# Kernel optimization log

Measured on AMD Instinct MI355X. Metric: run time of the kernel, lower is better.

The kernel has to match this reference:

```python
import jax, jax.numpy as jnp
import numpy as np

N = 100000
E = 1600000
IN, H, OUT = 128, 128, 64


def setup_inputs() -> dict:
    key = jax.random.key(0)
    k1, k2, k3, k4, k5, k6 = jax.random.split(key, 6)
    x = jax.random.normal(k1, (N, IN), dtype=jnp.float32)
    edge_index = jax.random.randint(k2, (2, E), 0, N, dtype=jnp.int64)
    W1 = jax.random.normal(k3, (IN, H), dtype=jnp.float32) / np.sqrt(IN)
    b1 = jnp.zeros((H,), dtype=jnp.float32)
    W2 = jax.random.normal(k4, (H, OUT), dtype=jnp.float32) / np.sqrt(H)
    b2 = jnp.zeros((OUT,), dtype=jnp.float32)
    return {"x": x, "edge_index": edge_index, "W1": W1, "b1": b1, "W2": W2, "b2": b2}


def gcn_conv(x, src, dst, W, b, num_nodes):
    # PyG GCNConv: linear transform, then symmetric-normalized aggregation
    h = x @ W                                         # (N, d_out)
    ones = jnp.ones(src.shape[0], dtype=h.dtype)
    deg = jax.ops.segment_sum(ones, dst, num_segments=num_nodes)  # in-degree incl. self-loops
    dis = jax.lax.rsqrt(jnp.maximum(deg, 1.0))        # deg >= 1 due to self-loops
    norm = dis[src] * dis[dst]                        # (E+N,)
    msg = h[src] * norm[:, None]                      # gather + scale (memory-bound)
    out = jax.ops.segment_sum(msg, dst, num_segments=num_nodes)
    return out + b


def reference(x, edge_index, W1, b1, W2, b2):
    loop = jnp.arange(N, dtype=edge_index.dtype)
    src = jnp.concatenate([edge_index[0], loop])
    dst = jnp.concatenate([edge_index[1], loop])
    h = gcn_conv(x, src, dst, W1, b1, N)
    h = jax.nn.relu(h)                                # dropout: eval mode (identity)
    out = gcn_conv(h, src, dst, W2, b2, N)
    return jax.nn.sigmoid(out) * 0.8 + 0.1
```

## Files before the change

### kernel.cpp

```cpp
#include <hip/hip_runtime.h>
#include <cstdint>
#include <cstddef>

#define IN_F 128
#define HID  128
#define OUTF 64

typedef unsigned int   uint32;
typedef unsigned short ushort16;

using frag_ab = __attribute__((ext_vector_type(8))) short;
using frag_cd = __attribute__((ext_vector_type(4))) float;

static constexpr int TPB = 256;
static constexpr int PT_TILE = 2048;
static constexpr int PT_EPT  = 8;
static constexpr int MAXBK   = 512;
static constexpr int MEGA_SMEM = 34816;

__device__ __forceinline__ float bflo(uint32 u) { return __uint_as_float(u << 16); }
__device__ __forceinline__ float bfhi(uint32 u) { return __uint_as_float(u & 0xFFFF0000u); }
__device__ __forceinline__ ushort16 f2bf(float f) {
    uint32 x = __float_as_uint(f);
    x = (x + 0x7FFFu + ((x >> 16) & 1u)) >> 16;
    return (ushort16)x;
}
__device__ __forceinline__ uint32 packbf(float a, float b) {
    return (uint32)f2bf(a) | ((uint32)f2bf(b) << 16);
}

__global__ void detect_i64_kernel(const uint32* __restrict__ p, int npairs, int* __restrict__ flag) {
    __shared__ int anynz;
    if (threadIdx.x == 0) anynz = 0;
    __syncthreads();
    int i = threadIdx.x;
    if (i < npairs && p[2 * i + 1] != 0u) atomicOr(&anynz, 1);
    __syncthreads();
    if (threadIdx.x == 0) *flag = (anynz == 0) ? 1 : 0;
}

__device__ __forceinline__ int load_idx(const void* p, int i, bool i64) {
    return i64 ? (int)((const long long*)p)[i] : ((const int*)p)[i];
}

__device__ void partition_body(char* smem, const void* __restrict__ ei, int E, bool i64,
                               int nbuckets, int bcap,
                               int* __restrict__ bcur, uint32* __restrict__ bbuf)
{
    uint32*   stash  = (uint32*)smem;
    ushort16* bidx   = (ushort16*)(smem + 8192);
    int*      hist   = (int*)(smem + 12288);
    int*      scanb  = (int*)(smem + 14336);
    int*      gbase  = (int*)(smem + 16384);
    int*      sum256 = (int*)(smem + 18432);

    int tile0 = blockIdx.x * PT_TILE;
    int tid = threadIdx.x;

    for (int i = tid; i < nbuckets; i += 256) hist[i] = 0;
    __syncthreads();

    uint32 pck[PT_EPT];
    int    lofs[PT_EPT];
    short  bkt[PT_EPT];
#pragma unroll
    for (int j = 0; j < PT_EPT; ++j) {
        int e = tile0 + j * 256 + tid;
        if (e < E) {
            int s = load_idx(ei, e, i64);
            int d = load_idx(ei, E + e, i64);
            int b = d >> 8;
            pck[j]  = (uint32)s | ((uint32)(d & 255) << 24);
            bkt[j]  = (short)b;
            lofs[j] = atomicAdd(&hist[b], 1);
        } else bkt[j] = -1;
    }
    __syncthreads();

    for (int i = tid; i < nbuckets; i += 256)
        gbase[i] = hist[i] ? atomicAdd(&bcur[i], hist[i]) : 0;

    {
        int lt = tid * 2;
        int h0 = 0, h1 = 0;
        if (lt + 0 < nbuckets) h0 = hist[lt + 0];
        if (lt + 1 < nbuckets) h1 = hist[lt + 1];
        int lsum = h0 + h1;
        sum256[tid] = lsum;
        __syncthreads();
        for (int off = 1; off < 256; off <<= 1) {
            int t = (tid >= off) ? sum256[tid - off] : 0;
            __syncthreads();
            sum256[tid] += t;
            __syncthreads();
        }
        int excl = sum256[tid] - lsum;
        if (lt + 0 < nbuckets) scanb[lt + 0] = excl;
        if (lt + 1 < nbuckets) scanb[lt + 1] = excl + h0;
    }
    __syncthreads();

#pragma unroll
    for (int j = 0; j < PT_EPT; ++j) {
        if (bkt[j] >= 0) {
            int p = scanb[bkt[j]] + lofs[j];
            stash[p] = pck[j];
            bidx[p]  = (ushort16)bkt[j];
        }
    }
    __syncthreads();

    int total = min(PT_TILE, E - tile0);
    for (int k = tid; k < total; k += 256) {
        int b = bidx[k];
        int dst = gbase[b] + (k - scanb[b]);
        if (dst < bcap) bbuf[(size_t)b * bcap + dst] = stash[k];
    }
}

__device__ void gemm1_body(char* smem, int gb, const float* __restrict__ X,
                           const float* __restrict__ W, ushort16* __restrict__ out, int M)
{
    typedef ushort16 WtRow[136];
    WtRow* Wt = (WtRow*)smem;

    for (int i = threadIdx.x; i < 128 * 128; i += 256) {
        int k = i >> 7, c = i & 127;
        Wt[c][k] = f2bf(W[i]);
    }
    __syncthreads();

    int wid  = threadIdx.x >> 6;
    int lane = threadIdx.x & 63;
    int g    = lane >> 4;
    int li   = lane & 15;

    int row = gb * 64 + wid * 16 + li;
    int rc  = min(row, M - 1);

    frag_cd acc[8];
#pragma unroll
    for (int i = 0; i < 8; ++i) acc[i] = (frag_cd)0.0f;

#pragma unroll
    for (int t = 0; t < 4; ++t) {
        const float* xp = X + (size_t)rc * 128 + t * 32 + g * 8;
        float4 p = *(const float4*)xp;
        float4 q = *(const float4*)(xp + 4);
        frag_ab a;
        a[0] = (short)f2bf(p.x); a[1] = (short)f2bf(p.y);
        a[2] = (short)f2bf(p.z); a[3] = (short)f2bf(p.w);
        a[4] = (short)f2bf(q.x); a[5] = (short)f2bf(q.y);
        a[6] = (short)f2bf(q.z); a[7] = (short)f2bf(q.w);
#pragma unroll
        for (int cb = 0; cb < 8; ++cb) {
            frag_ab b = *(const frag_ab*)&Wt[cb * 16 + li][t * 32 + g * 8];
            acc[cb] = __builtin_amdgcn_mfma_f32_16x16x32_bf16(a, b, acc[cb], 0, 0, 0);
        }
    }

    int ro = gb * 64 + wid * 16 + g * 4;
#pragma unroll
    for (int r = 0; r < 4; ++r) {
        int rr = ro + r;
        if (rr < M) {
#pragma unroll
            for (int cb = 0; cb < 8; ++cb)
                out[(size_t)rr * 128 + cb * 16 + li] = f2bf(acc[cb][r]);
        }
    }
}

__global__ __launch_bounds__(256) void mega1_kernel(
    const void* __restrict__ ei, int E, const int* __restrict__ flag,
    int nbuckets, int bcap, int* __restrict__ bcur, uint32* __restrict__ bbuf,
    const float* __restrict__ X, const float* __restrict__ W1,
    ushort16* __restrict__ H, int M, int PB)
{
    __shared__ char smem[MEGA_SMEM];
    if ((int)blockIdx.x < PB) {
        partition_body(smem, ei, E, (*flag != 0), nbuckets, bcap, bcur, bbuf);
    } else {
        gemm1_body(smem, blockIdx.x - PB, X, W1, H, M);
    }
}

__global__ void bucket_base_kernel(const int* __restrict__ bcur, int* __restrict__ bbase,
                                   int nbuckets, int bcap) {
    __shared__ int tmp[512];
    int tid = threadIdx.x;
    int v = (tid < nbuckets) ? min(bcur[tid], bcap) : 0;
    tmp[tid] = v;
    __syncthreads();
    for (int off = 1; off < 512; off <<= 1) {
        int t = (tid >= off) ? tmp[tid - off] : 0;
        __syncthreads();
        tmp[tid] += t;
        __syncthreads();
    }
    if (tid < nbuckets) bbase[tid] = tmp[tid] - v;
}

__global__ __launch_bounds__(256) void bucket_count2_kernel(
    const uint32* __restrict__ bbuf, const int* __restrict__ bcur, const int* __restrict__ bbase,
    int* __restrict__ counts, float* __restrict__ dis, int* __restrict__ row_ptr,
    int N, int bcap)
{
    __shared__ int h[256];
    __shared__ int sc[256];
    int tid = threadIdx.x;
    h[tid] = 0;
    __syncthreads();
    int b = blockIdx.x;
    int cnt = min(bcur[b], bcap);
    const uint32* src = bbuf + (size_t)b * bcap;
    for (int k = tid; k < cnt; k += 256) atomicAdd(&h[src[k] >> 24], 1);
    __syncthreads();
    int v = h[tid];
    sc[tid] = v;
    __syncthreads();
    for (int off = 1; off < 256; off <<= 1) {
        int t = (tid >= off) ? sc[tid - off] : 0;
        __syncthreads();
        sc[tid] += t;
        __syncthreads();
    }
    int node = (b << 8) + tid;
    if (node < N) {
        counts[node]  = v;
        dis[node]     = rsqrtf((float)(v + 1));
        row_ptr[node] = bbase[b] + sc[tid] - v;
    }
}

__global__ __launch_bounds__(256) void bucket_fill_kernel(
    const uint32* __restrict__ bbuf, const int* __restrict__ bcur,
    const int* __restrict__ row_ptr, int* __restrict__ csr, int N, int bcap)
{
    __shared__ int cur[256];
    int b = blockIdx.x;
    int node = (b << 8) + threadIdx.x;
    cur[threadIdx.x] = (node < N) ? row_ptr[node] : 0;
    __syncthreads();
    int cnt = min(bcur[b], bcap);
    const uint32* src = bbuf + (size_t)b * bcap;
    for (int k = threadIdx.x; k < cnt; k += 256) {
        uint32 p = src[k];
        int dl = p >> 24;
        int pos = atomicAdd(&cur[dl], 1);
        csr[pos] = (int)(p & 0xFFFFFF);
    }
}

__global__ void hist_kernel(const void* __restrict__ ei, int E, const int* __restrict__ flag,
                            int* __restrict__ counts) {
    int e = blockIdx.x * TPB + threadIdx.x;
    if (e >= E) return;
    bool i64 = (*flag != 0);
    atomicAdd(&counts[load_idx(ei, E + e, i64)], 1);
}

__global__ void fill_kernel(const void* __restrict__ ei, int E, const int* __restrict__ flag,
                            int* __restrict__ cursor, int* __restrict__ csr_src) {
    int e = blockIdx.x * TPB + threadIdx.x;
    if (e >= E) return;
    bool i64 = (*flag != 0);
    int s = load_idx(ei, e, i64);
    int d = load_idx(ei, E + e, i64);
    int pos = atomicAdd(&cursor[d], 1);
    csr_src[pos] = s;
}

__global__ void dis_kernel(const int* __restrict__ counts, float* __restrict__ dis, int n) {
    int i = blockIdx.x * TPB + threadIdx.x;
    if (i < n) dis[i] = rsqrtf((float)(counts[i] + 1));
}

__global__ void scan_block_kernel(const int* __restrict__ counts, int* __restrict__ excl,
                                  int* __restrict__ partials, int n) {
    __shared__ int tmp[TPB];
    int tid = threadIdx.x, gid = blockIdx.x * TPB + tid;
    int v = (gid < n) ? counts[gid] : 0;
    tmp[tid] = v;
    __syncthreads();
    for (int off = 1; off < TPB; off <<= 1) {
        int t = (tid >= off) ? tmp[tid - off] : 0;
        __syncthreads();
        tmp[tid] += t;
        __syncthreads();
    }
    if (gid < n) excl[gid] = tmp[tid] - v;
    if (tid == TPB - 1) partials[blockIdx.x] = tmp[TPB - 1];
}

__global__ void scan_partials_kernel(int* __restrict__ partials, int nb) {
    __shared__ int tmp[512];
    int tid = threadIdx.x;
    int v = (tid < nb) ? partials[tid] : 0;
    tmp[tid] = v;
    __syncthreads();
    for (int off = 1; off < 512; off <<= 1) {
        int t = (tid >= off) ? tmp[tid - off] : 0;
        __syncthreads();
        tmp[tid] += t;
        __syncthreads();
    }
    if (tid < nb) partials[tid] = tmp[tid] - v;
}

__global__ void add_offsets_kernel(int* __restrict__ excl, const int* __restrict__ partials,
                                   int* __restrict__ cursor, int n) {
    int i = blockIdx.x * TPB + threadIdx.x;
    if (i < n) {
        int v = excl[i] + partials[blockIdx.x];
        excl[i] = v;
        cursor[i] = v;
    }
}

template <int C, bool XBF, bool SCALE>
__global__ __launch_bounds__(256) void gemm_mfma_kernel(
    const void* __restrict__ Xv, const float* __restrict__ W,
    const float* __restrict__ dis, ushort16* __restrict__ out, int M)
{
    constexpr int NB = C / 16;
    __shared__ ushort16 Wt[C][136];

    for (int i = threadIdx.x; i < 128 * C; i += 256) {
        int k = i / C, c = i % C;
        Wt[c][k] = f2bf(W[i]);
    }
    __syncthreads();

    int wid  = threadIdx.x >> 6;
    int lane = threadIdx.x & 63;
    int g    = lane >> 4;
    int li   = lane & 15;

    int row = blockIdx.x * 64 + wid * 16 + li;
    int rc  = min(row, M - 1);

    frag_cd acc[NB];
#pragma unroll
    for (int i = 0; i < NB; ++i) acc[i] = (frag_cd)0.0f;

#pragma unroll
    for (int t = 0; t < 4; ++t) {
        frag_ab a;
        if (XBF) {
            const ushort16* xp = (const ushort16*)Xv + (size_t)rc * 128 + t * 32 + g * 8;
            a = *(const frag_ab*)xp;
        } else {
            const float* xp = (const float*)Xv + (size_t)rc * 128 + t * 32 + g * 8;
            float4 p = *(const float4*)xp;
            float4 q = *(const float4*)(xp + 4);
            a[0] = (short)f2bf(p.x); a[1] = (short)f2bf(p.y);
            a[2] = (short)f2bf(p.z); a[3] = (short)f2bf(p.w);
            a[4] = (short)f2bf(q.x); a[5] = (short)f2bf(q.y);
            a[6] = (short)f2bf(q.z); a[7] = (short)f2bf(q.w);
        }
#pragma unroll
        for (int cb = 0; cb < NB; ++cb) {
            frag_ab b = *(const frag_ab*)&Wt[cb * 16 + li][t * 32 + g * 8];
            acc[cb] = __builtin_amdgcn_mfma_f32_16x16x32_bf16(a, b, acc[cb], 0, 0, 0);
        }
    }

    int ro = blockIdx.x * 64 + wid * 16 + g * 4;
#pragma unroll
    for (int r = 0; r < 4; ++r) {
        int rr = ro + r;
        if (rr < M) {
            float dsc = SCALE ? dis[rr] : 1.0f;
#pragma unroll
            for (int cb = 0; cb < NB; ++cb)
                out[(size_t)rr * C + cb * 16 + li] = f2bf(acc[cb][r] * dsc);
        }
    }
}

#define ACC8(u, d) \
    a0 = fmaf(d, bflo(u.x), a0); a1 = fmaf(d, bfhi(u.x), a1); \
    a2 = fmaf(d, bflo(u.y), a2); a3 = fmaf(d, bfhi(u.y), a3); \
    a4 = fmaf(d, bflo(u.z), a4); a5 = fmaf(d, bfhi(u.z), a5); \
    a6 = fmaf(d, bflo(u.w), a6); a7 = fmaf(d, bfhi(u.w), a7);

__global__ __launch_bounds__(256) void agg128_kernel(
    const uint32* __restrict__ hs, const int* __restrict__ csr,
    const int* __restrict__ row_ptr, const int* __restrict__ counts,
    const float* __restrict__ dis, const float* __restrict__ b,
    uint32* __restrict__ out, int n)
{
    int wave = threadIdx.x >> 6;
    int lane = threadIdx.x & 63;
    int g    = lane >> 4;
    int sl   = lane & 15;
    int node = blockIdx.x * 4 + wave;
    if (node >= n) return;

    const uint4* hsv = (const uint4*)hs;
    float dsc = dis[node];
    float a0 = 0.f, a1 = 0.f, a2 = 0.f, a3 = 0.f,
          a4 = 0.f, a5 = 0.f, a6 = 0.f, a7 = 0.f;
    if (g == 0) {
        uint4 u = hsv[(size_t)node * 16 + sl];
        ACC8(u, dsc);
    }

    int start = row_ptr[node];
    int end   = start + counts[node];
    int k = start;
    for (; k + 15 < end; k += 16) {
        int base = k + (g << 2);
        int s0 = csr[base], s1 = csr[base + 1], s2 = csr[base + 2], s3 = csr[base + 3];
        float d0 = dis[s0], d1 = dis[s1], d2 = dis[s2], d3 = dis[s3];
        uint4 u0 = hsv[(size_t)s0 * 16 + sl];
        uint4 u1 = hsv[(size_t)s1 * 16 + sl];
        uint4 u2 = hsv[(size_t)s2 * 16 + sl];
        uint4 u3 = hsv[(size_t)s3 * 16 + sl];
        ACC8(u0, d0); ACC8(u1, d1); ACC8(u2, d2); ACC8(u3, d3);
    }
    for (; k + 7 < end; k += 8) {
        int base = k + (g << 1);
        int s0 = csr[base], s1 = csr[base + 1];
        float d0 = dis[s0], d1 = dis[s1];
        uint4 u0 = hsv[(size_t)s0 * 16 + sl];
        uint4 u1 = hsv[(size_t)s1 * 16 + sl];
        ACC8(u0, d0); ACC8(u1, d1);
    }
    for (; k < end; k += 4) {
        int e = k + g;
        if (e < end) {
            int s0 = csr[e];
            float d0 = dis[s0];
            uint4 u = hsv[(size_t)s0 * 16 + sl];
            ACC8(u, d0);
        }
    }

    a0 += __shfl_xor(a0, 16, 64); a0 += __shfl_xor(a0, 32, 64);
    a1 += __shfl_xor(a1, 16, 64); a1 += __shfl_xor(a1, 32, 64);
    a2 += __shfl_xor(a2, 16, 64); a2 += __shfl_xor(a2, 32, 64);
    a3 += __shfl_xor(a3, 16, 64); a3 += __shfl_xor(a3, 32, 64);
    a4 += __shfl_xor(a4, 16, 64); a4 += __shfl_xor(a4, 32, 64);
    a5 += __shfl_xor(a5, 16, 64); a5 += __shfl_xor(a5, 32, 64);
    a6 += __shfl_xor(a6, 16, 64); a6 += __shfl_xor(a6, 32, 64);
    a7 += __shfl_xor(a7, 16, 64); a7 += __shfl_xor(a7, 32, 64);

    if (g == 0) {
        float4 bb0 = ((const float4*)b)[sl * 2];
        float4 bb1 = ((const float4*)b)[sl * 2 + 1];
        float v0 = fmaxf(a0 * dsc + bb0.x, 0.0f);
        float v1 = fmaxf(a1 * dsc + bb0.y, 0.0f);
        float v2 = fmaxf(a2 * dsc + bb0.z, 0.0f);
        float v3 = fmaxf(a3 * dsc + bb0.w, 0.0f);
        float v4 = fmaxf(a4 * dsc + bb1.x, 0.0f);
        float v5 = fmaxf(a5 * dsc + bb1.y, 0.0f);
        float v6 = fmaxf(a6 * dsc + bb1.z, 0.0f);
        float v7 = fmaxf(a7 * dsc + bb1.w, 0.0f);
        uint4 o;
        o.x = packbf(v0, v1); o.y = packbf(v2, v3);
        o.z = packbf(v4, v5); o.w = packbf(v6, v7);
        ((uint4*)out)[(size_t)node * 16 + sl] = o;
    }
}

__global__ __launch_bounds__(256) void agg64_kernel(
    const uint32* __restrict__ hs, const int* __restrict__ csr,
    const int* __restrict__ row_ptr, const int* __restrict__ counts,
    const float* __restrict__ dis, const float* __restrict__ b,
    float* __restrict__ out, int n)
{
    int wave = threadIdx.x >> 6;
    int lane = threadIdx.x & 63;
    int g    = lane >> 3;
    int sl   = lane & 7;
    int node = blockIdx.x * 4 + wave;
    if (node >= n) return;

    const uint4* hsv = (const uint4*)hs;
    float a0 = 0.f, a1 = 0.f, a2 = 0.f, a3 = 0.f,
          a4 = 0.f, a5 = 0.f, a6 = 0.f, a7 = 0.f;
    if (g == 0) {
        uint4 u = hsv[(size_t)node * 8 + sl];
        ACC8(u, 1.0f);
    }

    int start = row_ptr[node];
    int end   = start + counts[node];
    int k = start;
    for (; k + 15 < end; k += 16) {
        int base = k + (g << 1);
        int s0 = csr[base], s1 = csr[base + 1];
        uint4 u0 = hsv[(size_t)s0 * 8 + sl];
        uint4 u1 = hsv[(size_t)s1 * 8 + sl];
        ACC8(u0, 1.0f); ACC8(u1, 1.0f);
    }
    for (; k + 7 < end; k += 8) {
        int e = k + g;
        uint4 u = hsv[(size_t)csr[e] * 8 + sl];
        ACC8(u, 1.0f);
    }
    for (; k < end; k += 8) {
        int e = k + g;
        if (e < end) {
            uint4 u = hsv[(size_t)csr[e] * 8 + sl];
            ACC8(u, 1.0f);
        }
    }

    a0 += __shfl_xor(a0, 8, 64); a0 += __shfl_xor(a0, 16, 64); a0 += __shfl_xor(a0, 32, 64);
    a1 += __shfl_xor(a1, 8, 64); a1 += __shfl_xor(a1, 16, 64); a1 += __shfl_xor(a1, 32, 64);
    a2 += __shfl_xor(a2, 8, 64); a2 += __shfl_xor(a2, 16, 64); a2 += __shfl_xor(a2, 32, 64);
    a3 += __shfl_xor(a3, 8, 64); a3 += __shfl_xor(a3, 16, 64); a3 += __shfl_xor(a3, 32, 64);
    a4 += __shfl_xor(a4, 8, 64); a4 += __shfl_xor(a4, 16, 64); a4 += __shfl_xor(a4, 32, 64);
    a5 += __shfl_xor(a5, 8, 64); a5 += __shfl_xor(a5, 16, 64); a5 += __shfl_xor(a5, 32, 64);
    a6 += __shfl_xor(a6, 8, 64); a6 += __shfl_xor(a6, 16, 64); a6 += __shfl_xor(a6, 32, 64);
    a7 += __shfl_xor(a7, 8, 64); a7 += __shfl_xor(a7, 16, 64); a7 += __shfl_xor(a7, 32, 64);

    if (g == 0) {
        float dsc = dis[node];
        float4 bb0 = ((const float4*)b)[sl * 2];
        float4 bb1 = ((const float4*)b)[sl * 2 + 1];
        float4 o0, o1;
        o0.x = 0.1f + 0.8f / (1.0f + __expf(-(a0 * dsc + bb0.x)));
        o0.y = 0.1f + 0.8f / (1.0f + __expf(-(a1 * dsc + bb0.y)));
        o0.z = 0.1f + 0.8f / (1.0f + __expf(-(a2 * dsc + bb0.z)));
        o0.w = 0.1f + 0.8f / (1.0f + __expf(-(a3 * dsc + bb0.w)));
        o1.x = 0.1f + 0.8f / (1.0f + __expf(-(a4 * dsc + bb1.x)));
        o1.y = 0.1f + 0.8f / (1.0f + __expf(-(a5 * dsc + bb1.y)));
        o1.z = 0.1f + 0.8f / (1.0f + __expf(-(a6 * dsc + bb1.z)));
        o1.w = 0.1f + 0.8f / (1.0f + __expf(-(a7 * dsc + bb1.w)));
        ((float4*)out)[(size_t)node * 16 + sl * 2]     = o0;
        ((float4*)out)[(size_t)node * 16 + sl * 2 + 1] = o1;
    }
}

extern "C" void kernel_launch(void* const* d_in, const int* in_sizes, int n_in,
                              void* d_out, int out_size, void* d_ws, size_t ws_size,
                              hipStream_t stream) {
    const float* x  = (const float*)d_in[0];
    const void*  ei = d_in[1];
    const float* W1 = (const float*)d_in[2];
    const float* b1 = (const float*)d_in[3];
    const float* W2 = (const float*)d_in[4];
    const float* b2 = (const float*)d_in[5];

    const int N = in_sizes[0] / IN_F;
    const int E = in_sizes[1] / 2;

    const int nbuckets = (N + 255) >> 8;
    const int bcap     = (int)(2 * ((long long)E / (nbuckets > 0 ? nbuckets : 1)) + 2048);
    const bool bucketed = (nbuckets <= MAXBK);

    auto alignup = [](size_t v) { return (v + 255) & ~(size_t)255; };
    char* w = (char*)d_ws;
    size_t off = 0;
    int*      flag     = (int*)(w + off);      off = alignup(off + 16);
    int*      counts   = (int*)(w + off);      off = alignup(off + (size_t)(N + MAXBK) * sizeof(int));
    int*      bcur     = counts + N;
    int*      bbase    = (int*)(w + off);      off = alignup(off + MAXBK * sizeof(int));
    int*      cursor   = (int*)(w + off);      off = alignup(off + (size_t)N * sizeof(int));
    int*      row_ptr  = (int*)(w + off);      off = alignup(off + (size_t)N * sizeof(int));
    int*      partials = (int*)(w + off);      off = alignup(off + 512 * sizeof(int));
    float*    dis      = (float*)(w + off);    off = alignup(off + (size_t)N * sizeof(float));
    int*      csr      = (int*)(w + off);      off = alignup(off + (size_t)E * sizeof(int));
    uint32*   bbuf     = (uint32*)(w + off);   off = alignup(off + (size_t)nbuckets * bcap * sizeof(uint32));
    uint32*   A        = (uint32*)(w + off);   off = alignup(off + (size_t)N * HID * sizeof(ushort16));
    uint32*   B        = (uint32*)(w + off);   off = alignup(off + (size_t)N * HID * sizeof(ushort16));

    const int nbN = (N + TPB - 1) / TPB;
    const int nbE = (E + TPB - 1) / TPB;
    const int gemmBlocks = (N + 63) / 64;

    detect_i64_kernel<<<1, TPB, 0, stream>>>((const uint32*)ei, 256, flag);

    if (bucketed) {
        hipMemsetAsync(bcur, 0, MAXBK * sizeof(int), stream);
        const int PB = (E + PT_TILE - 1) / PT_TILE;
        mega1_kernel<<<PB + gemmBlocks, TPB, 0, stream>>>(
            ei, E, flag, nbuckets, bcap, bcur, bbuf, x, W1, (ushort16*)A, N, PB);
        bucket_base_kernel<<<1, 512, 0, stream>>>(bcur, bbase, nbuckets, bcap);
        bucket_count2_kernel<<<nbuckets, TPB, 0, stream>>>(bbuf, bcur, bbase, counts, dis, row_ptr, N, bcap);
        bucket_fill_kernel<<<nbuckets, TPB, 0, stream>>>(bbuf, bcur, row_ptr, csr, N, bcap);
    } else {
        hipMemsetAsync(counts, 0, (size_t)(N + MAXBK) * sizeof(int), stream);
        hist_kernel<<<nbE, TPB, 0, stream>>>(ei, E, flag, counts);
        dis_kernel<<<nbN, TPB, 0, stream>>>(counts, dis, N);
        scan_block_kernel<<<nbN, TPB, 0, stream>>>(counts, row_ptr, partials, N);
        scan_partials_kernel<<<1, 512, 0, stream>>>(partials, nbN);
        add_offsets_kernel<<<nbN, TPB, 0, stream>>>(row_ptr, partials, cursor, N);
        fill_kernel<<<nbE, TPB, 0, stream>>>(ei, E, flag, cursor, csr);
        gemm_mfma_kernel<HID, false, false><<<gemmBlocks, TPB, 0, stream>>>(x, W1, dis, (ushort16*)A, N);
    }

    agg128_kernel<<<(N + 3) / 4, TPB, 0, stream>>>(A, csr, row_ptr, counts, dis, b1, B, N);

    gemm_mfma_kernel<OUTF, true, true><<<gemmBlocks, TPB, 0, stream>>>(B, W2, dis, (ushort16*)A, N);
    agg64_kernel<<<(N + 3) / 4, TPB, 0, stream>>>(A, csr, row_ptr, counts, dis, b2, (float*)d_out, N);
}
```

Measured before the change: 203.3 us.

## Pre-transpose weights once, merge bucket scan/count/fill kernels, fold memset into prep

```diff
diff --git a/kernel.cpp b/kernel.cpp
--- a/kernel.cpp
+++ b/kernel.cpp
@@ -16,7 +16,7 @@
 static constexpr int PT_TILE = 2048;
 static constexpr int PT_EPT  = 8;
 static constexpr int MAXBK   = 512;
-static constexpr int MEGA_SMEM = 34816;
+static constexpr int PART_SMEM = 19456;
 
 __device__ __forceinline__ float bflo(uint32 u) { return __uint_as_float(u << 16); }
 __device__ __forceinline__ float bfhi(uint32 u) { return __uint_as_float(u & 0xFFFF0000u); }
@@ -29,18 +29,98 @@
     return (uint32)f2bf(a) | ((uint32)f2bf(b) << 16);
 }
 
-__global__ void detect_i64_kernel(const uint32* __restrict__ p, int npairs, int* __restrict__ flag) {
-    __shared__ int anynz;
-    if (threadIdx.x == 0) anynz = 0;
-    __syncthreads();
-    int i = threadIdx.x;
-    if (i < npairs && p[2 * i + 1] != 0u) atomicOr(&anynz, 1);
-    __syncthreads();
-    if (threadIdx.x == 0) *flag = (anynz == 0) ? 1 : 0;
-}
-
 __device__ __forceinline__ int load_idx(const void* p, int i, bool i64) {
     return i64 ? (int)((const long long*)p)[i] : ((const int*)p)[i];
+}
+
+__global__ void prep_kernel(const uint32* __restrict__ p, int* __restrict__ flag,
+                            int* __restrict__ bcur,
+                            const float* __restrict__ W1, const float* __restrict__ W2,
+                            ushort16* __restrict__ W1t, ushort16* __restrict__ W2t)
+{
+    int tid = threadIdx.x;
+    if (blockIdx.x == 0) {
+        __shared__ int anynz;
+        if (tid == 0) anynz = 0;
+        __syncthreads();
+        if (p[2 * tid + 1] != 0u) atomicOr(&anynz, 1);
+        bcur[tid] = 0; bcur[tid + 256] = 0;
+        __syncthreads();
+        if (tid == 0) *flag = (anynz == 0) ? 1 : 0;
+        return;
+    }
+    int i = (blockIdx.x - 1) * TPB + tid;
+    if (i < 128 * 128) {
+        int k = i >> 7, c = i & 127;
+        W1t[c * 128 + k] = f2bf(W1[i]);
+    } else {
+        int j = i - 128 * 128;
+        if (j < 128 * 64) {
+            int k = j >> 6, c = j & 63;
+            W2t[c * 128 + k] = f2bf(W2[j]);
+        }
+    }
+}
+
+template <int C, bool XBF, bool SCALE>
+__device__ __forceinline__ void gemm_global_body(
+    int gb, const void* __restrict__ Xv, const ushort16* __restrict__ Wt,
+    const float* __restrict__ dis, ushort16* __restrict__ out, int M)
+{
+    constexpr int NB = C / 16;
+    int wid  = threadIdx.x >> 6;
+    int lane = threadIdx.x & 63;
+    int g    = lane >> 4;
+    int li   = lane & 15;
+
+    int row = gb * 64 + wid * 16 + li;
+    int rc  = min(row, M - 1);
+
+    frag_cd acc[NB];
+#pragma unroll
+    for (int i = 0; i < NB; ++i) acc[i] = (frag_cd)0.0f;
+
+#pragma unroll
+    for (int t = 0; t < 4; ++t) {
+        frag_ab a;
+        if (XBF) {
+            const ushort16* xp = (const ushort16*)Xv + (size_t)rc * 128 + t * 32 + g * 8;
+            a = *(const frag_ab*)xp;
+        } else {
+            const float* xp = (const float*)Xv + (size_t)rc * 128 + t * 32 + g * 8;
+            float4 pp = *(const float4*)xp;
+            float4 qq = *(const float4*)(xp + 4);
+            a[0] = (short)f2bf(pp.x); a[1] = (short)f2bf(pp.y);
+            a[2] = (short)f2bf(pp.z); a[3] = (short)f2bf(pp.w);
+            a[4] = (short)f2bf(qq.x); a[5] = (short)f2bf(qq.y);
+            a[6] = (short)f2bf(qq.z); a[7] = (short)f2bf(qq.w);
+        }
+#pragma unroll
+        for (int cb = 0; cb < NB; ++cb) {
+            frag_ab b = *(const frag_ab*)&Wt[(size_t)(cb * 16 + li) * 128 + t * 32 + g * 8];
+            acc[cb] = __builtin_amdgcn_mfma_f32_16x16x32_bf16(a, b, acc[cb], 0, 0, 0);
+        }
+    }
+
+    int ro = gb * 64 + wid * 16 + g * 4;
+#pragma unroll
+    for (int r = 0; r < 4; ++r) {
+        int rr = ro + r;
+        if (rr < M) {
+            float dsc = SCALE ? dis[rr] : 1.0f;
+#pragma unroll
+            for (int cb = 0; cb < NB; ++cb)
+                out[(size_t)rr * C + cb * 16 + li] = f2bf(acc[cb][r] * dsc);
+        }
+    }
+}
+
+template <int C, bool XBF, bool SCALE>
+__global__ __launch_bounds__(256) void gemm_global_kernel(
+    const void* __restrict__ Xv, const ushort16* __restrict__ Wt,
+    const float* __restrict__ dis, ushort16* __restrict__ out, int M)
+{
+    gemm_global_body<C, XBF, SCALE>(blockIdx.x, Xv, Wt, dis, out, M);
 }
 
 __device__ void partition_body(char* smem, const void* __restrict__ ei, int E, bool i64,
@@ -118,104 +198,55 @@
     }
 }
 
-__device__ void gemm1_body(char* smem, int gb, const float* __restrict__ X,
-                           const float* __restrict__ W, ushort16* __restrict__ out, int M)
-{
-    typedef ushort16 WtRow[136];
-    WtRow* Wt = (WtRow*)smem;
-
-    for (int i = threadIdx.x; i < 128 * 128; i += 256) {
-        int k = i >> 7, c = i & 127;
-        Wt[c][k] = f2bf(W[i]);
-    }
-    __syncthreads();
-
-    int wid  = threadIdx.x >> 6;
-    int lane = threadIdx.x & 63;
-    int g    = lane >> 4;
-    int li   = lane & 15;
-
-    int row = gb * 64 + wid * 16 + li;
-    int rc  = min(row, M - 1);
-
-    frag_cd acc[8];
-#pragma unroll
-    for (int i = 0; i < 8; ++i) acc[i] = (frag_cd)0.0f;
-
-#pragma unroll
-    for (int t = 0; t < 4; ++t) {
-        const float* xp = X + (size_t)rc * 128 + t * 32 + g * 8;
-        float4 p = *(const float4*)xp;
-        float4 q = *(const float4*)(xp + 4);
-        frag_ab a;
-        a[0] = (short)f2bf(p.x); a[1] = (short)f2bf(p.y);
-        a[2] = (short)f2bf(p.z); a[3] = (short)f2bf(p.w);
-        a[4] = (short)f2bf(q.x); a[5] = (short)f2bf(q.y);
-        a[6] = (short)f2bf(q.z); a[7] = (short)f2bf(q.w);
-#pragma unroll
-        for (int cb = 0; cb < 8; ++cb) {
-            frag_ab b = *(const frag_ab*)&Wt[cb * 16 + li][t * 32 + g * 8];
-            acc[cb] = __builtin_amdgcn_mfma_f32_16x16x32_bf16(a, b, acc[cb], 0, 0, 0);
-        }
-    }
-
-    int ro = gb * 64 + wid * 16 + g * 4;
-#pragma unroll
-    for (int r = 0; r < 4; ++r) {
-        int rr = ro + r;
-        if (rr < M) {
-#pragma unroll
-            for (int cb = 0; cb < 8; ++cb)
-                out[(size_t)rr * 128 + cb * 16 + li] = f2bf(acc[cb][r]);
-        }
-    }
-}
-
 __global__ __launch_bounds__(256) void mega1_kernel(
     const void* __restrict__ ei, int E, const int* __restrict__ flag,
     int nbuckets, int bcap, int* __restrict__ bcur, uint32* __restrict__ bbuf,
-    const float* __restrict__ X, const float* __restrict__ W1,
+    const float* __restrict__ X, const ushort16* __restrict__ W1t,
     ushort16* __restrict__ H, int M, int PB)
 {
-    __shared__ char smem[MEGA_SMEM];
+    __shared__ char smem[PART_SMEM];
     if ((int)blockIdx.x < PB) {
         partition_body(smem, ei, E, (*flag != 0), nbuckets, bcap, bcur, bbuf);
     } else {
-        gemm1_body(smem, blockIdx.x - PB, X, W1, H, M);
-    }
-}
-
-__global__ void bucket_base_kernel(const int* __restrict__ bcur, int* __restrict__ bbase,
-                                   int nbuckets, int bcap) {
-    __shared__ int tmp[512];
-    int tid = threadIdx.x;
-    int v = (tid < nbuckets) ? min(bcur[tid], bcap) : 0;
-    tmp[tid] = v;
-    __syncthreads();
-    for (int off = 1; off < 512; off <<= 1) {
-        int t = (tid >= off) ? tmp[tid - off] : 0;
-        __syncthreads();
-        tmp[tid] += t;
-        __syncthreads();
-    }
-    if (tid < nbuckets) bbase[tid] = tmp[tid] - v;
-}
-
-__global__ __launch_bounds__(256) void bucket_count2_kernel(
-    const uint32* __restrict__ bbuf, const int* __restrict__ bcur, const int* __restrict__ bbase,
+        gemm_global_body<HID, false, false>(blockIdx.x - PB, X, W1t, nullptr, H, M);
+    }
+}
+
+__global__ __launch_bounds__(256) void bucket_build_kernel(
+    const uint32* __restrict__ bbuf, const int* __restrict__ bcur,
     int* __restrict__ counts, float* __restrict__ dis, int* __restrict__ row_ptr,
-    int N, int bcap)
-{
+    int* __restrict__ csr, int N, int nbuckets, int bcap)
+{
+    __shared__ int pcnt[512];
+    __shared__ int pinc[256];
     __shared__ int h[256];
     __shared__ int sc[256];
+    __shared__ int cur[256];
+
     int tid = threadIdx.x;
+    int b = blockIdx.x;
+
+    pcnt[tid]       = (tid < nbuckets)       ? min(bcur[tid], bcap)       : 0;
+    pcnt[tid + 256] = (tid + 256 < nbuckets) ? min(bcur[tid + 256], bcap) : 0;
     h[tid] = 0;
     __syncthreads();
-    int b = blockIdx.x;
+    int ps = pcnt[2 * tid] + pcnt[2 * tid + 1];
+    pinc[tid] = ps;
+    __syncthreads();
+    for (int off = 1; off < 256; off <<= 1) {
+        int t = (tid >= off) ? pinc[tid - off] : 0;
+        __syncthreads();
+        pinc[tid] += t;
+        __syncthreads();
+    }
+    int p2 = b >> 1;
+    int bbase = pinc[p2] - (pcnt[2 * p2] + pcnt[2 * p2 + 1]) + ((b & 1) ? pcnt[b - 1] : 0);
+
     int cnt = min(bcur[b], bcap);
     const uint32* src = bbuf + (size_t)b * bcap;
     for (int k = tid; k < cnt; k += 256) atomicAdd(&h[src[k] >> 24], 1);
     __syncthreads();
+
     int v = h[tid];
     sc[tid] = v;
     __syncthreads();
@@ -225,26 +256,17 @@
         sc[tid] += t;
         __syncthreads();
     }
+    int myrow = bbase + sc[tid] - v;
     int node = (b << 8) + tid;
     if (node < N) {
         counts[node]  = v;
         dis[node]     = rsqrtf((float)(v + 1));
-        row_ptr[node] = bbase[b] + sc[tid] - v;
-    }
-}
-
-__global__ __launch_bounds__(256) void bucket_fill_kernel(
-    const uint32* __restrict__ bbuf, const int* __restrict__ bcur,
-    const int* __restrict__ row_ptr, int* __restrict__ csr, int N, int bcap)
-{
-    __shared__ int cur[256];
-    int b = blockIdx.x;
-    int node = (b << 8) + threadIdx.x;
-    cur[threadIdx.x] = (node < N) ? row_ptr[node] : 0;
-    __syncthreads();
-    int cnt = min(bcur[b], bcap);
-    const uint32* src = bbuf + (size_t)b * bcap;
-    for (int k = threadIdx.x; k < cnt; k += 256) {
+        row_ptr[node] = myrow;
+    }
+    cur[tid] = myrow;
+    __syncthreads();
+
+    for (int k = tid; k < cnt; k += 256) {
         uint32 p = src[k];
         int dl = p >> 24;
         int pos = atomicAdd(&cur[dl], 1);
@@ -315,67 +337,6 @@
         int v = excl[i] + partials[blockIdx.x];
         excl[i] = v;
         cursor[i] = v;
-    }
-}
-
-template <int C, bool XBF, bool SCALE>
-__global__ __launch_bounds__(256) void gemm_mfma_kernel(
-    const void* __restrict__ Xv, const float* __restrict__ W,
-    const float* __restrict__ dis, ushort16* __restrict__ out, int M)
-{
-    constexpr int NB = C / 16;
-    __shared__ ushort16 Wt[C][136];
-
-    for (int i = threadIdx.x; i < 128 * C; i += 256) {
-        int k = i / C, c = i % C;
-        Wt[c][k] = f2bf(W[i]);
-    }
-    __syncthreads();
-
-    int wid  = threadIdx.x >> 6;
-    int lane = threadIdx.x & 63;
-    int g    = lane >> 4;
-    int li   = lane & 15;
-
-    int row = blockIdx.x * 64 + wid * 16 + li;
-    int rc  = min(row, M - 1);
-
-    frag_cd acc[NB];
-#pragma unroll
-    for (int i = 0; i < NB; ++i) acc[i] = (frag_cd)0.0f;
-
-#pragma unroll
-    for (int t = 0; t < 4; ++t) {
-        frag_ab a;
-        if (XBF) {
-            const ushort16* xp = (const ushort16*)Xv + (size_t)rc * 128 + t * 32 + g * 8;
-            a = *(const frag_ab*)xp;
-        } else {
-            const float* xp = (const float*)Xv + (size_t)rc * 128 + t * 32 + g * 8;
-            float4 p = *(const float4*)xp;
-            float4 q = *(const float4*)(xp + 4);
-            a[0] = (short)f2bf(p.x); a[1] = (short)f2bf(p.y);
-            a[2] = (short)f2bf(p.z); a[3] = (short)f2bf(p.w);
-            a[4] = (short)f2bf(q.x); a[5] = (short)f2bf(q.y);
-            a[6] = (short)f2bf(q.z); a[7] = (short)f2bf(q.w);
-        }
-#pragma unroll
-        for (int cb = 0; cb < NB; ++cb) {
-            frag_ab b = *(const frag_ab*)&Wt[cb * 16 + li][t * 32 + g * 8];
-            acc[cb] = __builtin_amdgcn_mfma_f32_16x16x32_bf16(a, b, acc[cb], 0, 0, 0);
-        }
-    }
-
-    int ro = blockIdx.x * 64 + wid * 16 + g * 4;
-#pragma unroll
-    for (int r = 0; r < 4; ++r) {
-        int rr = ro + r;
-        if (rr < M) {
-            float dsc = SCALE ? dis[rr] : 1.0f;
-#pragma unroll
-            for (int cb = 0; cb < NB; ++cb)
-                out[(size_t)rr * C + cb * 16 + li] = f2bf(acc[cb][r] * dsc);
-        }
     }
 }
 
@@ -559,7 +520,8 @@
     int*      flag     = (int*)(w + off);      off = alignup(off + 16);
     int*      counts   = (int*)(w + off);      off = alignup(off + (size_t)(N + MAXBK) * sizeof(int));
     int*      bcur     = counts + N;
-    int*      bbase    = (int*)(w + off);      off = alignup(off + MAXBK * sizeof(int));
+    ushort16* W1t      = (ushort16*)(w + off); off = alignup(off + 128 * 128 * sizeof(ushort16));
+    ushort16* W2t      = (ushort16*)(w + off); off = alignup(off + 64 * 128 * sizeof(ushort16));
     int*      cursor   = (int*)(w + off);      off = alignup(off + (size_t)N * sizeof(int));
     int*      row_ptr  = (int*)(w + off);      off = alignup(off + (size_t)N * sizeof(int));
     int*      partials = (int*)(w + off);      off = alignup(off + 512 * sizeof(int));
@@ -572,17 +534,16 @@
     const int nbN = (N + TPB - 1) / TPB;
     const int nbE = (E + TPB - 1) / TPB;
     const int gemmBlocks = (N + 63) / 64;
-
-    detect_i64_kernel<<<1, TPB, 0, stream>>>((const uint32*)ei, 256, flag);
+    const int prepBlocks = 1 + (128 * 128 + 128 * 64 + TPB - 1) / TPB;
+
+    prep_kernel<<<prepBlocks, TPB, 0, stream>>>((const uint32*)ei, flag, bcur, W1, W2, W1t, W2t);
 
     if (bucketed) {
-        hipMemsetAsync(bcur, 0, MAXBK * sizeof(int), stream);
         const int PB = (E + PT_TILE - 1) / PT_TILE;
         mega1_kernel<<<PB + gemmBlocks, TPB, 0, stream>>>(
-            ei, E, flag, nbuckets, bcap, bcur, bbuf, x, W1, (ushort16*)A, N, PB);
-        bucket_base_kernel<<<1, 512, 0, stream>>>(bcur, bbase, nbuckets, bcap);
-        bucket_count2_kernel<<<nbuckets, TPB, 0, stream>>>(bbuf, bcur, bbase, counts, dis, row_ptr, N, bcap);
-        bucket_fill_kernel<<<nbuckets, TPB, 0, stream>>>(bbuf, bcur, row_ptr, csr, N, bcap);
+            ei, E, flag, nbuckets, bcap, bcur, bbuf, x, W1t, (ushort16*)A, N, PB);
+        bucket_build_kernel<<<nbuckets, TPB, 0, stream>>>(
+            bbuf, bcur, counts, dis, row_ptr, csr, N, nbuckets, bcap);
     } else {
         hipMemsetAsync(counts, 0, (size_t)(N + MAXBK) * sizeof(int), stream);
         hist_kernel<<<nbE, TPB, 0, stream>>>(ei, E, flag, counts);
@@ -591,11 +552,11 @@
         scan_partials_kernel<<<1, 512, 0, stream>>>(partials, nbN);
         add_offsets_kernel<<<nbN, TPB, 0, stream>>>(row_ptr, partials, cursor, N);
         fill_kernel<<<nbE, TPB, 0, stream>>>(ei, E, flag, cursor, csr);
-        gemm_mfma_kernel<HID, false, false><<<gemmBlocks, TPB, 0, stream>>>(x, W1, dis, (ushort16*)A, N);
+        gemm_global_kernel<HID, false, false><<<gemmBlocks, TPB, 0, stream>>>(x, W1t, dis, (ushort16*)A, N);
     }
 
     agg128_kernel<<<(N + 3) / 4, TPB, 0, stream>>>(A, csr, row_ptr, counts, dis, b1, B, N);
 
-    gemm_mfma_kernel<OUTF, true, true><<<gemmBlocks, TPB, 0, stream>>>(B, W2, dis, (ushort16*)A, N);
+    gemm_global_kernel<OUTF, true, true><<<gemmBlocks, TPB, 0, stream>>>(B, W2t, dis, (ushort16*)A, N);
     agg64_kernel<<<(N + 3) / 4, TPB, 0, stream>>>(A, csr, row_ptr, counts, dis, b2, (float*)d_out, N);
 }
```

After: 222.0 us. +9.2%, slower.
